# Performance work log

Measured on AMD Instinct MI355X. Metric: run time of the kernel, lower is better.

## Reference

```python
import jax, jax.numpy as jnp
import numpy as np

N_NODES, IN_DIM, HID, LAT, N_EDGES = 50000, 3000, 512, 30, 800000
NEG_SLOPE = 0.2


def setup_inputs() -> dict:
    key = jax.random.key(0)
    ks = jax.random.split(key, 6)
    x = jax.random.normal(ks[0], (N_NODES, IN_DIM), dtype=jnp.float32)
    edge_index = jax.random.randint(ks[1], (2, N_EDGES), 0, N_NODES, dtype=jnp.int64)
    # xavier-normal-ish scales
    W1 = jax.random.normal(ks[2], (IN_DIM, HID), dtype=jnp.float32) * 0.02
    W2 = jax.random.normal(ks[3], (HID, LAT), dtype=jnp.float32) * 0.06
    att_src = jax.random.normal(ks[4], (HID,), dtype=jnp.float32) * 0.1
    att_dst = jax.random.normal(ks[5], (HID,), dtype=jnp.float32) * 0.1
    return {"x": x, "edge_index": edge_index, "W1": W1, "W2": W2,
            "att_src": att_src, "att_dst": att_dst}


def _segment_softmax(e, seg, num_segments):
    # numerically stable softmax over variable-degree dst neighborhoods
    m = jax.ops.segment_max(e, seg, num_segments=num_segments)
    m = jnp.where(jnp.isfinite(m), m, 0.0)  # empty segments -> 0, harmless
    p = jnp.exp(e - m[seg])
    s = jax.ops.segment_sum(p, seg, num_segments=num_segments)
    return p / (s[seg] + 1e-16)


def reference(x, edge_index, W1, W2, att_src, att_dst):
    N = x.shape[0]
    src, dst = edge_index[0], edge_index[1]  # messages flow src(j) -> dst(i)

    # ---- conv1: full GAT layer (heads=1, no self-loops, no bias) ----
    h1 = x @ W1                                   # [N, 512]
    a_src = h1 @ att_src                          # [N]
    a_dst = h1 @ att_dst                          # [N]
    e = jax.nn.leaky_relu(a_src[src] + a_dst[dst], NEG_SLOPE)  # [E]
    alpha = _segment_softmax(e, dst, N)           # [E] (also tied attn for conv3)
    agg1 = jax.ops.segment_sum(h1[src] * alpha[:, None], dst, num_segments=N)
    x1 = jax.nn.elu(agg1)                         # [N, 512]

    # ---- conv2: attention=False -> plain linear projection ----
    x2 = x1 @ W2                                  # [N, 30] (latent embedding)

    # ---- conv3: tied weights (W2^T) + tied attention from conv1 ----
    h3 = x2 @ W2.T                                # [N, 512]
    agg3 = jax.ops.segment_sum(h3[src] * alpha[:, None], dst, num_segments=N)
    x3 = jax.nn.elu(agg3)

    # ---- conv4: attention=False, tied weights (W1^T) ----
    x4 = x3 @ W1.T                                # [N, in_channels]
    return (x2, x4)
```

## Files before the change

### kernel.cpp

```cpp
#include <hip/hip_runtime.h>

#define N_NODES 50000
#define IN_DIM  3000
#define HID     512
#define LAT     30
#define N_EDGES 800000
#define M_PAD   50048
#define K1_PAD  3008
#define N4_PAD  3072

typedef __bf16 bf16;
typedef unsigned int uint;
typedef __attribute__((ext_vector_type(4))) float f32x4;
typedef __attribute__((ext_vector_type(8))) bf16 bf16x8;

__device__ __forceinline__ float bf2f(bf16 b){ return (float)b; }

__device__ __forceinline__ void gl16(const void* g, void* l){
  __builtin_amdgcn_global_load_lds(
      (const __attribute__((address_space(1))) void*)g,
      (__attribute__((address_space(3))) void*)l, 16, 0, 0);
}

__global__ void k_w1t(const float* __restrict__ W1, bf16* __restrict__ W1T){
  int k = blockIdx.x*256 + threadIdx.x;
  int n = blockIdx.y;
  if (k >= K1_PAD) return;
  float v = (k < IN_DIM) ? W1[(long)k*HID + n] : 0.f;
  W1T[(long)n*K1_PAD + k] = (bf16)v;
}
__global__ void k_w1p(const float* __restrict__ W1, bf16* __restrict__ W1P){
  int k = blockIdx.x*256 + threadIdx.x;
  int n = blockIdx.y;
  if (k >= HID) return;
  float v = (n < IN_DIM) ? W1[(long)n*HID + k] : 0.f;
  W1P[(long)n*HID + k] = (bf16)v;
}
__global__ void k_w2t(const float* __restrict__ W2, bf16* __restrict__ W2T){
  int k = blockIdx.x*256 + threadIdx.x;
  int n = blockIdx.y;
  if (k >= HID) return;
  float v = (n < LAT) ? W2[(long)k*LAT + n] : 0.f;
  W2T[(long)n*HID + k] = (bf16)v;
}
__global__ void k_w2p(const float* __restrict__ W2, bf16* __restrict__ W2P){
  int t = blockIdx.x*256 + threadIdx.x;
  if (t >= HID*32) return;
  int n = t >> 5, k = t & 31;
  W2P[t] = (bf16)((k < LAT) ? W2[(long)n*LAT + k] : 0.f);
}

__global__ __launch_bounds__(256) void k_cvt(const float* __restrict__ x, bf16* __restrict__ xb){
  int chunk = blockIdx.x*256 + threadIdx.x;
  int row = blockIdx.y;
  if (chunk >= K1_PAD/8) return;
  int c8 = chunk*8;
  bf16x8 o;
  if (row < N_NODES && c8 + 8 <= IN_DIM){
    float4 v0 = *(const float4*)(x + (long)row*IN_DIM + c8);
    float4 v1 = *(const float4*)(x + (long)row*IN_DIM + c8 + 4);
    o[0]=(bf16)v0.x; o[1]=(bf16)v0.y; o[2]=(bf16)v0.z; o[3]=(bf16)v0.w;
    o[4]=(bf16)v1.x; o[5]=(bf16)v1.y; o[6]=(bf16)v1.z; o[7]=(bf16)v1.w;
  } else {
    #pragma unroll
    for (int j=0;j<8;j++){
      int c = c8 + j;
      float v = (row < N_NODES && c < IN_DIM) ? x[(long)row*IN_DIM + c] : 0.f;
      o[j] = (bf16)v;
    }
  }
  *(bf16x8*)(xb + (long)row*K1_PAD + c8) = o;
}

template<bool C_F32, bool ELU>
__global__ __launch_bounds__(256) void gemm_glds(
    const bf16* __restrict__ A, const bf16* __restrict__ B, void* __restrict__ Cp,
    int lda, int ldb, int Ksteps, int Mvalid, int Nvalid, int ldc)
{
  __shared__ bf16 Alds[128*32];
  __shared__ bf16 Blds[128*32];
  const int tid  = threadIdx.x;
  const int lane = tid & 63;
  const int w    = tid >> 6;
  const int wm   = (w >> 1) * 64, wn = (w & 1) * 64;
  const int col0 = blockIdx.x * 128, row0 = blockIdx.y * 128;

  f32x4 acc[4][4];
  #pragma unroll
  for (int mi=0;mi<4;mi++)
    #pragma unroll
    for (int ni=0;ni<4;ni++)
      acc[mi][ni] = (f32x4){0.f,0.f,0.f,0.f};

  const int sr = tid >> 2;
  const int sc = (tid & 3) * 16;

  const char* ga = (const char*)(A + (long)(row0 + sr) * lda) + sc;
  const char* gb = (const char*)(B + (long)(col0 + sr) * ldb) + sc;
  char* la = (char*)Alds + sr*64 + sc;
  char* lb = (char*)Blds + sr*64 + sc;
  const long astep = (long)64 * lda * 2;
  const long bstep = (long)64 * ldb * 2;

  for (int ks = 0; ks < Ksteps; ks++){
    const long ko = (long)ks * 64;
    gl16(ga + ko,         la);
    gl16(ga + ko + astep, la + 64*64);
    gl16(gb + ko,         lb);
    gl16(gb + ko + bstep, lb + 64*64);
    __syncthreads();

    bf16x8 af[4], bfr[4];
    #pragma unroll
    for (int mi=0;mi<4;mi++)
      af[mi] = *(const bf16x8*)&Alds[(wm + mi*16 + (lane & 15))*32 + (lane>>4)*8];
    #pragma unroll
    for (int ni=0;ni<4;ni++)
      bfr[ni] = *(const bf16x8*)&Blds[(wn + ni*16 + (lane & 15))*32 + (lane>>4)*8];
    #pragma unroll
    for (int mi=0;mi<4;mi++)
      #pragma unroll
      for (int ni=0;ni<4;ni++)
        acc[mi][ni] = __builtin_amdgcn_mfma_f32_16x16x32_bf16(af[mi], bfr[ni], acc[mi][ni], 0, 0, 0);
    __syncthreads();
  }

  const int crb  = (lane >> 4) * 4;
  const int ccol = lane & 15;
  #pragma unroll
  for (int mi=0;mi<4;mi++){
    #pragma unroll
    for (int v=0;v<4;v++){
      int r = row0 + wm + mi*16 + crb + v;
      if (r >= Mvalid) continue;
      #pragma unroll
      for (int ni=0;ni<4;ni++){
        int c = col0 + wn + ni*16 + ccol;
        if (c >= Nvalid) continue;
        float val = acc[mi][ni][v];
        if (ELU) val = (val > 0.f) ? val : expm1f(val);
        if (C_F32) ((float*)Cp)[(long)r*ldc + c] = val;
        else       ((bf16*)Cp)[(long)r*ldc + c] = (bf16)val;
      }
    }
  }
}

__global__ void k_attdots(const bf16* __restrict__ h1, const float* __restrict__ att_s,
                          const float* __restrict__ att_d, float* __restrict__ a_src,
                          float* __restrict__ a_dst){
  int gid = blockIdx.x * blockDim.x + threadIdx.x;
  int row = gid >> 6, lane = gid & 63;
  if (row >= N_NODES) return;
  bf16x8 hv = *(const bf16x8*)(h1 + (long)row*HID + lane*8);
  float s1 = 0.f, s2 = 0.f;
  #pragma unroll
  for (int j=0;j<8;j++){
    float h = bf2f(hv[j]);
    s1 = fmaf(h, att_s[lane*8+j], s1);
    s2 = fmaf(h, att_d[lane*8+j], s2);
  }
  #pragma unroll
  for (int o=32;o>0;o>>=1){ s1 += __shfl_down(s1,o); s2 += __shfl_down(s2,o); }
  if (lane == 0){ a_src[row] = s1; a_dst[row] = s2; }
}

__global__ void k_deg(const int* __restrict__ ei, int* __restrict__ deg){
  int e = blockIdx.x*256 + threadIdx.x;
  if (e >= N_EDGES) return;
  atomicAdd(&deg[ei[N_EDGES + e]], 1);
}

__global__ void k_scan(const int* __restrict__ deg, int* __restrict__ off, int* __restrict__ cur){
  const int n = M_PAD, T = 1024;
  int t = threadIdx.x;
  const int per = (n + T - 1) / T;
  int s0 = t*per, s1 = min(n, s0+per);
  int sum = 0;
  for (int i=s0;i<s1;i++) sum += deg[i];
  __shared__ int sd[1024];
  sd[t] = sum; __syncthreads();
  for (int o=1;o<T;o<<=1){
    int x = (t>=o) ? sd[t-o] : 0;
    __syncthreads();
    sd[t] += x;
    __syncthreads();
  }
  int run = sd[t] - sum;
  for (int i=s0;i<s1;i++){
    off[i] = run; cur[i] = run;
    run += deg[i];
  }
  if (s0 < n && s1 == n) off[n] = run;
}

__global__ void k_fill(const int* __restrict__ ei, int* __restrict__ cur, int* __restrict__ csr_src){
  int e = blockIdx.x*256 + threadIdx.x;
  if (e >= N_EDGES) return;
  int d = ei[N_EDGES + e];
  int pos = atomicAdd(&cur[d], 1);
  csr_src[pos] = ei[e];
}

__global__ __launch_bounds__(512) void k_conv1(
    const int* __restrict__ off, const int* __restrict__ csr_src,
    const float* __restrict__ a_src, const float* __restrict__ a_dst,
    const bf16* __restrict__ h1, bf16* __restrict__ x1,
    float* __restrict__ p_edge, float* __restrict__ s_node)
{
  const int i = blockIdx.x;
  const int t = threadIdx.x;
  const int start = off[i];
  const int deg = off[i+1] - start;
  __shared__ float p_sh[512];
  __shared__ int   s_sh[512];
  __shared__ float red[512];

  const float ad = a_dst[i];
  float mloc = -1e30f;
  for (int base=0; base<deg; base+=512){
    int k = base + t;
    if (k < deg){
      float e = a_src[csr_src[start+k]] + ad;
      e = (e > 0.f) ? e : 0.2f*e;
      mloc = fmaxf(mloc, e);
    }
  }
  red[t] = mloc; __syncthreads();
  for (int o=256;o>0;o>>=1){ if (t<o) red[t] = fmaxf(red[t], red[t+o]); __syncthreads(); }
  const float m = red[0];
  __syncthreads();

  float acc = 0.f, ssum = 0.f;
  for (int base=0; base<deg; base+=512){
    int cnt = min(512, deg-base);
    if (t < cnt){
      int s = csr_src[start+base+t];
      float e = a_src[s] + ad;
      e = (e > 0.f) ? e : 0.2f*e;
      float p = __expf(e - m);
      p_sh[t] = p; s_sh[t] = s;
      p_edge[start+base+t] = p;
    }
    __syncthreads();
    for (int k=0;k<cnt;k++){
      float pk = p_sh[k];
      ssum += pk;
      acc = fmaf(pk, bf2f(h1[(long)s_sh[k]*HID + t]), acc);
    }
    __syncthreads();
  }
  float val = acc / (ssum + 1e-16f);
  val = (val > 0.f) ? val : expm1f(val);
  x1[(long)i*HID + t] = (bf16)val;
  if (t == 0) s_node[i] = ssum;
}

__global__ void k_agg3(const int* __restrict__ off, const int* __restrict__ csr_src,
                       const float* __restrict__ p_edge, const float* __restrict__ s_node,
                       const float* __restrict__ x2, bf16* __restrict__ aggb)
{
  int i = blockIdx.x*8 + (threadIdx.x >> 5);
  int lane = threadIdx.x & 31;
  if (i >= M_PAD) return;
  float acc = 0.f;
  if (i < N_NODES){
    int s0 = off[i], d = off[i+1] - s0;
    for (int k=0;k<d;k++){
      int s = csr_src[s0+k];
      float pk = p_edge[s0+k];
      if (lane < LAT) acc = fmaf(pk, x2[(long)s*LAT + lane], acc);
    }
    acc *= 1.f/(s_node[i] + 1e-16f);
  }
  aggb[(long)i*32 + lane] = (bf16)((lane < LAT) ? acc : 0.f);
}

extern "C" void kernel_launch(void* const* d_in, const int* in_sizes, int n_in,
                              void* d_out, int out_size, void* d_ws, size_t ws_size,
                              hipStream_t stream)
{
  const float* x     = (const float*)d_in[0];
  const int*   ei    = (const int*)d_in[1];
  const float* W1    = (const float*)d_in[2];
  const float* W2    = (const float*)d_in[3];
  const float* att_s = (const float*)d_in[4];
  const float* att_d = (const float*)d_in[5];

  float* out_x2 = (float*)d_out;
  float* out_x4 = (float*)d_out + (long)N_NODES*LAT;

  bf16* xb = (bf16*)out_x4;
  bf16* h1 = xb + (long)M_PAD*K1_PAD;
  bf16* x1 = h1 + (long)M_PAD*HID;

  char* w = (char*)d_ws;
  bf16* W1T = (bf16*)w;  w += (long)HID*K1_PAD*2;
  bf16* W1P = (bf16*)w;  w += (long)N4_PAD*HID*2;
  bf16* W2T = (bf16*)w;  w += (long)128*HID*2;
  bf16* W2P = (bf16*)w;  w += (long)HID*32*2;
  bf16* x3  = (bf16*)w;  w += (long)M_PAD*HID*2;
  bf16* aggb= (bf16*)w;  w += (long)M_PAD*32*2;
  int* deg  = (int*)w;   w += (long)M_PAD*4;
  int* offs = (int*)w;   w += (long)(M_PAD+64)*4;
  int* cur  = (int*)w;   w += (long)M_PAD*4;
  int* csr  = (int*)w;   w += (long)N_EDGES*4;
  float* p_e = (float*)w; w += (long)N_EDGES*4;
  float* s_n = (float*)w; w += (long)M_PAD*4;
  float* a_s = (float*)w; w += (long)M_PAD*4;
  float* a_d = (float*)w; w += (long)M_PAD*4;

  k_w1t<<<dim3((K1_PAD+255)/256, HID), 256, 0, stream>>>(W1, W1T);
  k_w1p<<<dim3((HID+255)/256, N4_PAD), 256, 0, stream>>>(W1, W1P);
  k_w2t<<<dim3(2, 128), 256, 0, stream>>>(W2, W2T);
  k_w2p<<<(HID*32+255)/256, 256, 0, stream>>>(W2, W2P);
  k_cvt<<<dim3((K1_PAD/8+255)/256, M_PAD), 256, 0, stream>>>(x, xb);

  hipMemsetAsync(deg, 0, (size_t)M_PAD*4, stream);
  k_deg<<<(N_EDGES+255)/256, 256, 0, stream>>>(ei, deg);
  k_scan<<<1, 1024, 0, stream>>>(deg, offs, cur);
  k_fill<<<(N_EDGES+255)/256, 256, 0, stream>>>(ei, cur, csr);

  gemm_glds<false,false><<<dim3(HID/128, M_PAD/128), 256, 0, stream>>>(
      xb, W1T, h1, K1_PAD, K1_PAD, K1_PAD/32, M_PAD, HID, HID);

  k_attdots<<<(N_NODES*64)/256, 256, 0, stream>>>(h1, att_s, att_d, a_s, a_d);

  k_conv1<<<M_PAD, 512, 0, stream>>>(offs, csr, a_s, a_d, h1, x1, p_e, s_n);

  gemm_glds<true,false><<<dim3(1, M_PAD/128), 256, 0, stream>>>(
      x1, W2T, out_x2, HID, HID, HID/32, N_NODES, LAT, LAT);

  k_agg3<<<(M_PAD+7)/8, 256, 0, stream>>>(offs, csr, p_e, s_n, out_x2, aggb);
  gemm_glds<false,true><<<dim3(HID/128, M_PAD/128), 256, 0, stream>>>(
      aggb, W2P, x3, 32, 32, 1, M_PAD, HID, HID);

  gemm_glds<true,false><<<dim3(N4_PAD/128, M_PAD/128), 256, 0, stream>>>(
      x3, W1P, out_x4, HID, HID, HID/32, N_NODES, IN_DIM, IN_DIM);
}
```

Baseline: 1.335 ms.

## Fuse fp32-to-bf16 conversion into GEMM1, precompute edge exps, swizzle workgroups across XCDs

```diff
diff --git a/kernel.cpp b/kernel.cpp
--- a/kernel.cpp
+++ b/kernel.cpp
@@ -22,6 +22,12 @@
       (__attribute__((address_space(3))) void*)l, 16, 0, 0);
 }
 
+__device__ __forceinline__ int xcd_swz(int orig, int nwg){
+  int q = nwg >> 3, r = nwg & 7;
+  int xcd = orig & 7, lid = orig >> 3;
+  return (xcd < r ? xcd*(q+1) : r*(q+1) + (xcd-r)*q) + lid;
+}
+
 __global__ void k_w1t(const float* __restrict__ W1, bf16* __restrict__ W1T){
   int k = blockIdx.x*256 + threadIdx.x;
   int n = blockIdx.y;
@@ -50,32 +56,115 @@
   W2P[t] = (bf16)((k < LAT) ? W2[(long)n*LAT + k] : 0.f);
 }
 
-__global__ __launch_bounds__(256) void k_cvt(const float* __restrict__ x, bf16* __restrict__ xb){
-  int chunk = blockIdx.x*256 + threadIdx.x;
-  int row = blockIdx.y;
-  if (chunk >= K1_PAD/8) return;
-  int c8 = chunk*8;
-  bf16x8 o;
-  if (row < N_NODES && c8 + 8 <= IN_DIM){
-    float4 v0 = *(const float4*)(x + (long)row*IN_DIM + c8);
-    float4 v1 = *(const float4*)(x + (long)row*IN_DIM + c8 + 4);
-    o[0]=(bf16)v0.x; o[1]=(bf16)v0.y; o[2]=(bf16)v0.z; o[3]=(bf16)v0.w;
-    o[4]=(bf16)v1.x; o[5]=(bf16)v1.y; o[6]=(bf16)v1.z; o[7]=(bf16)v1.w;
-  } else {
-    #pragma unroll
-    for (int j=0;j<8;j++){
-      int c = c8 + j;
-      float v = (row < N_NODES && c < IN_DIM) ? x[(long)row*IN_DIM + c] : 0.f;
-      o[j] = (bf16)v;
-    }
-  }
-  *(bf16x8*)(xb + (long)row*K1_PAD + c8) = o;
+__global__ __launch_bounds__(256) void gemm_a32(
+    const float* __restrict__ X, const bf16* __restrict__ Bw, bf16* __restrict__ C)
+{
+  __shared__ bf16 Alds[2][128*32];
+  __shared__ bf16 Blds[2][128*32];
+  const int NBX = HID/128;
+  const int tid  = threadIdx.x;
+  const int lane = tid & 63;
+  const int w    = tid >> 6;
+  const int wm   = (w >> 1) * 64, wn = (w & 1) * 64;
+  const int wgid = xcd_swz(blockIdx.x, gridDim.x);
+  const int col0 = (wgid % NBX) * 128, row0 = (wgid / NBX) * 128;
+  const int Ksteps = K1_PAD/32;
+
+  f32x4 acc[4][4];
+  #pragma unroll
+  for (int mi=0;mi<4;mi++)
+    #pragma unroll
+    for (int ni=0;ni<4;ni++)
+      acc[mi][ni] = (f32x4){0.f,0.f,0.f,0.f};
+
+  const int arow = tid >> 1;
+  const int cg   = (tid & 1) * 16;
+  const float* pA = X + (long)min(row0 + arow, N_NODES-1) * IN_DIM;
+
+  const int sr = tid >> 2;
+  const int sc = (tid & 3) * 16;
+  const char* gB = (const char*)(Bw + (long)(col0 + sr) * K1_PAD) + sc;
+  const long bstep = (long)64 * K1_PAD * 2;
+  char* lB0 = (char*)&Blds[0][0] + sr*64 + sc;
+  char* lB1 = (char*)&Blds[1][0] + sr*64 + sc;
+
+  {
+    int kb = cg;
+    float4 q0 = *(const float4*)(pA + kb);
+    float4 q1 = *(const float4*)(pA + kb + 4);
+    float4 q2 = *(const float4*)(pA + kb + 8);
+    float4 q3 = *(const float4*)(pA + kb + 12);
+    gl16(gB, lB0);
+    gl16(gB + bstep, lB0 + 64*64);
+    bf16x8 v0, v1;
+    v0[0]=(bf16)q0.x; v0[1]=(bf16)q0.y; v0[2]=(bf16)q0.z; v0[3]=(bf16)q0.w;
+    v0[4]=(bf16)q1.x; v0[5]=(bf16)q1.y; v0[6]=(bf16)q1.z; v0[7]=(bf16)q1.w;
+    v1[0]=(bf16)q2.x; v1[1]=(bf16)q2.y; v1[2]=(bf16)q2.z; v1[3]=(bf16)q2.w;
+    v1[4]=(bf16)q3.x; v1[5]=(bf16)q3.y; v1[6]=(bf16)q3.z; v1[7]=(bf16)q3.w;
+    *(bf16x8*)&Alds[0][arow*32 + cg]     = v0;
+    *(bf16x8*)&Alds[0][arow*32 + cg + 8] = v1;
+  }
+
+  for (int ks = 0; ks < Ksteps; ks++){
+    const int c = ks & 1;
+    __syncthreads();
+    const bool pf = (ks+1 < Ksteps);
+    float4 q0,q1,q2,q3;
+    if (pf){
+      int kb = (ks+1)*32 + cg;
+      q0 = *(const float4*)(pA + min(kb,      IN_DIM-4));
+      q1 = *(const float4*)(pA + min(kb + 4,  IN_DIM-4));
+      q2 = *(const float4*)(pA + min(kb + 8,  IN_DIM-4));
+      q3 = *(const float4*)(pA + min(kb + 12, IN_DIM-4));
+      const char* g = gB + (long)(ks+1)*64;
+      char* l = c ? lB0 : lB1;
+      gl16(g, l);
+      gl16(g + bstep, l + 64*64);
+    }
+    bf16x8 af[4], bfr[4];
+    #pragma unroll
+    for (int mi=0;mi<4;mi++)
+      af[mi] = *(const bf16x8*)&Alds[c][(wm + mi*16 + (lane & 15))*32 + (lane>>4)*8];
+    #pragma unroll
+    for (int ni=0;ni<4;ni++)
+      bfr[ni] = *(const bf16x8*)&Blds[c][(wn + ni*16 + (lane & 15))*32 + (lane>>4)*8];
+    #pragma unroll
+    for (int mi=0;mi<4;mi++)
+      #pragma unroll
+      for (int ni=0;ni<4;ni++)
+        acc[mi][ni] = __builtin_amdgcn_mfma_f32_16x16x32_bf16(af[mi], bfr[ni], acc[mi][ni], 0, 0, 0);
+    if (pf){
+      bf16x8 v0, v1;
+      v0[0]=(bf16)q0.x; v0[1]=(bf16)q0.y; v0[2]=(bf16)q0.z; v0[3]=(bf16)q0.w;
+      v0[4]=(bf16)q1.x; v0[5]=(bf16)q1.y; v0[6]=(bf16)q1.z; v0[7]=(bf16)q1.w;
+      v1[0]=(bf16)q2.x; v1[1]=(bf16)q2.y; v1[2]=(bf16)q2.z; v1[3]=(bf16)q2.w;
+      v1[4]=(bf16)q3.x; v1[5]=(bf16)q3.y; v1[6]=(bf16)q3.z; v1[7]=(bf16)q3.w;
+      *(bf16x8*)&Alds[c^1][arow*32 + cg]     = v0;
+      *(bf16x8*)&Alds[c^1][arow*32 + cg + 8] = v1;
+    }
+  }
+
+  const int crb  = (lane >> 4) * 4;
+  const int ccol = lane & 15;
+  #pragma unroll
+  for (int mi=0;mi<4;mi++){
+    #pragma unroll
+    for (int v=0;v<4;v++){
+      int r = row0 + wm + mi*16 + crb + v;
+      if (r >= N_NODES) continue;
+      #pragma unroll
+      for (int ni=0;ni<4;ni++){
+        int cc = col0 + wn + ni*16 + ccol;
+        C[(long)r*HID + cc] = (bf16)acc[mi][ni][v];
+      }
+    }
+  }
 }
 
 template<bool C_F32, bool ELU>
 __global__ __launch_bounds__(256) void gemm_glds(
     const bf16* __restrict__ A, const bf16* __restrict__ B, void* __restrict__ Cp,
-    int lda, int ldb, int Ksteps, int Mvalid, int Nvalid, int ldc)
+    int lda, int ldb, int Ksteps, int Mvalid, int Nvalid, int ldc, int NBX)
 {
   __shared__ bf16 Alds[128*32];
   __shared__ bf16 Blds[128*32];
@@ -83,7 +172,8 @@
   const int lane = tid & 63;
   const int w    = tid >> 6;
   const int wm   = (w >> 1) * 64, wn = (w & 1) * 64;
-  const int col0 = blockIdx.x * 128, row0 = blockIdx.y * 128;
+  const int wgid = xcd_swz(blockIdx.x, gridDim.x);
+  const int col0 = (wgid % NBX) * 128, row0 = (wgid / NBX) * 128;
 
   f32x4 acc[4][4];
   #pragma unroll
@@ -194,19 +284,25 @@
   if (s0 < n && s1 == n) off[n] = run;
 }
 
-__global__ void k_fill(const int* __restrict__ ei, int* __restrict__ cur, int* __restrict__ csr_src){
+__global__ void k_fill(const int* __restrict__ ei, int* __restrict__ cur,
+                       int* __restrict__ csr_src, const float* __restrict__ a_s,
+                       const float* __restrict__ a_d, float* __restrict__ p_e){
   int e = blockIdx.x*256 + threadIdx.x;
   if (e >= N_EDGES) return;
+  int s = ei[e];
   int d = ei[N_EDGES + e];
   int pos = atomicAdd(&cur[d], 1);
-  csr_src[pos] = ei[e];
-}
-
-__global__ __launch_bounds__(512) void k_conv1(
+  csr_src[pos] = s;
+  float v = a_s[s] + a_d[d];
+  v = (v > 0.f) ? v : 0.2f*v;
+  p_e[pos] = __expf(v);
+}
+
+__global__ __launch_bounds__(512) void k_agg1(
     const int* __restrict__ off, const int* __restrict__ csr_src,
-    const float* __restrict__ a_src, const float* __restrict__ a_dst,
+    const float* __restrict__ p_edge,
     const bf16* __restrict__ h1, bf16* __restrict__ x1,
-    float* __restrict__ p_edge, float* __restrict__ s_node)
+    float* __restrict__ s_node)
 {
   const int i = blockIdx.x;
   const int t = threadIdx.x;
@@ -214,33 +310,13 @@
   const int deg = off[i+1] - start;
   __shared__ float p_sh[512];
   __shared__ int   s_sh[512];
-  __shared__ float red[512];
-
-  const float ad = a_dst[i];
-  float mloc = -1e30f;
-  for (int base=0; base<deg; base+=512){
-    int k = base + t;
-    if (k < deg){
-      float e = a_src[csr_src[start+k]] + ad;
-      e = (e > 0.f) ? e : 0.2f*e;
-      mloc = fmaxf(mloc, e);
-    }
-  }
-  red[t] = mloc; __syncthreads();
-  for (int o=256;o>0;o>>=1){ if (t<o) red[t] = fmaxf(red[t], red[t+o]); __syncthreads(); }
-  const float m = red[0];
-  __syncthreads();
 
   float acc = 0.f, ssum = 0.f;
   for (int base=0; base<deg; base+=512){
     int cnt = min(512, deg-base);
     if (t < cnt){
-      int s = csr_src[start+base+t];
-      float e = a_src[s] + ad;
-      e = (e > 0.f) ? e : 0.2f*e;
-      float p = __expf(e - m);
-      p_sh[t] = p; s_sh[t] = s;
-      p_edge[start+base+t] = p;
+      p_sh[t] = p_edge[start+base+t];
+      s_sh[t] = csr_src[start+base+t];
     }
     __syncthreads();
     for (int k=0;k<cnt;k++){
@@ -290,8 +366,7 @@
   float* out_x2 = (float*)d_out;
   float* out_x4 = (float*)d_out + (long)N_NODES*LAT;
 
-  bf16* xb = (bf16*)out_x4;
-  bf16* h1 = xb + (long)M_PAD*K1_PAD;
+  bf16* h1 = (bf16*)out_x4;
   bf16* x1 = h1 + (long)M_PAD*HID;
 
   char* w = (char*)d_ws;
@@ -314,27 +389,26 @@
   k_w1p<<<dim3((HID+255)/256, N4_PAD), 256, 0, stream>>>(W1, W1P);
   k_w2t<<<dim3(2, 128), 256, 0, stream>>>(W2, W2T);
   k_w2p<<<(HID*32+255)/256, 256, 0, stream>>>(W2, W2P);
-  k_cvt<<<dim3((K1_PAD/8+255)/256, M_PAD), 256, 0, stream>>>(x, xb);
 
   hipMemsetAsync(deg, 0, (size_t)M_PAD*4, stream);
   k_deg<<<(N_EDGES+255)/256, 256, 0, stream>>>(ei, deg);
   k_scan<<<1, 1024, 0, stream>>>(deg, offs, cur);
-  k_fill<<<(N_EDGES+255)/256, 256, 0, stream>>>(ei, cur, csr);
-
-  gemm_glds<false,false><<<dim3(HID/128, M_PAD/128), 256, 0, stream>>>(
-      xb, W1T, h1, K1_PAD, K1_PAD, K1_PAD/32, M_PAD, HID, HID);
+
+  gemm_a32<<<(M_PAD/128)*(HID/128), 256, 0, stream>>>(x, W1T, h1);
 
   k_attdots<<<(N_NODES*64)/256, 256, 0, stream>>>(h1, att_s, att_d, a_s, a_d);
 
-  k_conv1<<<M_PAD, 512, 0, stream>>>(offs, csr, a_s, a_d, h1, x1, p_e, s_n);
-
-  gemm_glds<true,false><<<dim3(1, M_PAD/128), 256, 0, stream>>>(
-      x1, W2T, out_x2, HID, HID, HID/32, N_NODES, LAT, LAT);
+  k_fill<<<(N_EDGES+255)/256, 256, 0, stream>>>(ei, cur, csr, a_s, a_d, p_e);
+
+  k_agg1<<<N_NODES, 512, 0, stream>>>(offs, csr, p_e, h1, x1, s_n);
+
+  gemm_glds<true,false><<<1*(M_PAD/128), 256, 0, stream>>>(
+      x1, W2T, out_x2, HID, HID, HID/32, N_NODES, LAT, LAT, 1);
 
   k_agg3<<<(M_PAD+7)/8, 256, 0, stream>>>(offs, csr, p_e, s_n, out_x2, aggb);
-  gemm_glds<false,true><<<dim3(HID/128, M_PAD/128), 256, 0, stream>>>(
-      aggb, W2P, x3, 32, 32, 1, M_PAD, HID, HID);
-
-  gemm_glds<true,false><<<dim3(N4_PAD/128, M_PAD/128), 256, 0, stream>>>(
-      x3, W1P, out_x4, HID, HID, HID/32, N_NODES, IN_DIM, IN_DIM);
-}
+  gemm_glds<false,true><<<(HID/128)*(M_PAD/128), 256, 0, stream>>>(
+      aggb, W2P, x3, 32, 32, 1, M_PAD, HID, HID, HID/128);
+
+  gemm_glds<true,false><<<(N4_PAD/128)*(M_PAD/128), 256, 0, stream>>>(
+      x3, W1P, out_x4, HID, HID, HID/32, N_NODES, IN_DIM, IN_DIM, N4_PAD/128);
+}
```

New measurement: 1.362 ms. 2.1% more time.

## Double-buffer GEMM LDS loads, swizzle XCD tiles, precompute edge exps in fill

Applied to the files above, without the earlier changes.

```diff
diff --git a/kernel.cpp b/kernel.cpp
--- a/kernel.cpp
+++ b/kernel.cpp
@@ -20,6 +20,12 @@
   __builtin_amdgcn_global_load_lds(
       (const __attribute__((address_space(1))) void*)g,
       (__attribute__((address_space(3))) void*)l, 16, 0, 0);
+}
+
+__device__ __forceinline__ int xcd_swz(int orig, int nwg){
+  int q = nwg >> 3, r = nwg & 7;
+  int xcd = orig & 7, lid = orig >> 3;
+  return (xcd < r ? xcd*(q+1) : r*(q+1) + (xcd-r)*q) + lid;
 }
 
 __global__ void k_w1t(const float* __restrict__ W1, bf16* __restrict__ W1T){
@@ -75,15 +81,16 @@
 template<bool C_F32, bool ELU>
 __global__ __launch_bounds__(256) void gemm_glds(
     const bf16* __restrict__ A, const bf16* __restrict__ B, void* __restrict__ Cp,
-    int lda, int ldb, int Ksteps, int Mvalid, int Nvalid, int ldc)
+    int lda, int ldb, int Ksteps, int Mvalid, int Nvalid, int ldc, int NBX)
 {
-  __shared__ bf16 Alds[128*32];
-  __shared__ bf16 Blds[128*32];
+  __shared__ bf16 Alds[2][128*32];
+  __shared__ bf16 Blds[2][128*32];
   const int tid  = threadIdx.x;
   const int lane = tid & 63;
   const int w    = tid >> 6;
   const int wm   = (w >> 1) * 64, wn = (w & 1) * 64;
-  const int col0 = blockIdx.x * 128, row0 = blockIdx.y * 128;
+  const int wgid = xcd_swz(blockIdx.x, gridDim.x);
+  const int col0 = (wgid % NBX) * 128, row0 = (wgid / NBX) * 128;
 
   f32x4 acc[4][4];
   #pragma unroll
@@ -94,36 +101,51 @@
 
   const int sr = tid >> 2;
   const int sc = (tid & 3) * 16;
-
   const char* ga = (const char*)(A + (long)(row0 + sr) * lda) + sc;
   const char* gb = (const char*)(B + (long)(col0 + sr) * ldb) + sc;
-  char* la = (char*)Alds + sr*64 + sc;
-  char* lb = (char*)Blds + sr*64 + sc;
   const long astep = (long)64 * lda * 2;
   const long bstep = (long)64 * ldb * 2;
 
+#define STAGE_G(buf, ks) do{                                            \
+    const long ko_ = (long)(ks) * 64;                                   \
+    char* la_ = (char*)&Alds[buf][0] + sr*64 + sc;                      \
+    char* lb_ = (char*)&Blds[buf][0] + sr*64 + sc;                      \
+    gl16(ga + ko_,         la_);                                        \
+    gl16(ga + ko_ + astep, la_ + 64*64);                                \
+    gl16(gb + ko_,         lb_);                                        \
+    gl16(gb + ko_ + bstep, lb_ + 64*64);                                \
+  }while(0)
+
+  STAGE_G(0, 0);
+
   for (int ks = 0; ks < Ksteps; ks++){
-    const long ko = (long)ks * 64;
-    gl16(ga + ko,         la);
-    gl16(ga + ko + astep, la + 64*64);
-    gl16(gb + ko,         lb);
-    gl16(gb + ko + bstep, lb + 64*64);
-    __syncthreads();
-
+    const int cur = ks & 1;
+    if (ks + 1 < Ksteps){
+      STAGE_G(cur^1, ks+1);
+      asm volatile("s_waitcnt vmcnt(4)" ::: "memory");
+    } else {
+      asm volatile("s_waitcnt vmcnt(0)" ::: "memory");
+    }
+    __builtin_amdgcn_s_barrier();
+
+    const bf16* Ac = &Alds[cur][0];
+    const bf16* Bc = &Blds[cur][0];
     bf16x8 af[4], bfr[4];
     #pragma unroll
     for (int mi=0;mi<4;mi++)
-      af[mi] = *(const bf16x8*)&Alds[(wm + mi*16 + (lane & 15))*32 + (lane>>4)*8];
+      af[mi] = *(const bf16x8*)&Ac[(wm + mi*16 + (lane & 15))*32 + (lane>>4)*8];
     #pragma unroll
     for (int ni=0;ni<4;ni++)
-      bfr[ni] = *(const bf16x8*)&Blds[(wn + ni*16 + (lane & 15))*32 + (lane>>4)*8];
+      bfr[ni] = *(const bf16x8*)&Bc[(wn + ni*16 + (lane & 15))*32 + (lane>>4)*8];
     #pragma unroll
     for (int mi=0;mi<4;mi++)
       #pragma unroll
       for (int ni=0;ni<4;ni++)
         acc[mi][ni] = __builtin_amdgcn_mfma_f32_16x16x32_bf16(af[mi], bfr[ni], acc[mi][ni], 0, 0, 0);
-    __syncthreads();
-  }
+
+    __builtin_amdgcn_s_barrier();
+  }
+#undef STAGE_G
 
   const int crb  = (lane >> 4) * 4;
   const int ccol = lane & 15;
@@ -194,19 +216,25 @@
   if (s0 < n && s1 == n) off[n] = run;
 }
 
-__global__ void k_fill(const int* __restrict__ ei, int* __restrict__ cur, int* __restrict__ csr_src){
+__global__ void k_fill(const int* __restrict__ ei, int* __restrict__ cur,
+                       int* __restrict__ csr_src, const float* __restrict__ a_s,
+                       const float* __restrict__ a_d, float* __restrict__ p_e){
   int e = blockIdx.x*256 + threadIdx.x;
   if (e >= N_EDGES) return;
+  int s = ei[e];
   int d = ei[N_EDGES + e];
   int pos = atomicAdd(&cur[d], 1);
-  csr_src[pos] = ei[e];
-}
-
-__global__ __launch_bounds__(512) void k_conv1(
+  csr_src[pos] = s;
+  float v = a_s[s] + a_d[d];
+  v = (v > 0.f) ? v : 0.2f*v;
+  p_e[pos] = __expf(v);
+}
+
+__global__ __launch_bounds__(512) void k_agg1(
     const int* __restrict__ off, const int* __restrict__ csr_src,
-    const float* __restrict__ a_src, const float* __restrict__ a_dst,
+    const float* __restrict__ p_edge,
     const bf16* __restrict__ h1, bf16* __restrict__ x1,
-    float* __restrict__ p_edge, float* __restrict__ s_node)
+    float* __restrict__ s_node)
 {
   const int i = blockIdx.x;
   const int t = threadIdx.x;
@@ -214,33 +242,13 @@
   const int deg = off[i+1] - start;
   __shared__ float p_sh[512];
   __shared__ int   s_sh[512];
-  __shared__ float red[512];
-
-  const float ad = a_dst[i];
-  float mloc = -1e30f;
-  for (int base=0; base<deg; base+=512){
-    int k = base + t;
-    if (k < deg){
-      float e = a_src[csr_src[start+k]] + ad;
-      e = (e > 0.f) ? e : 0.2f*e;
-      mloc = fmaxf(mloc, e);
-    }
-  }
-  red[t] = mloc; __syncthreads();
-  for (int o=256;o>0;o>>=1){ if (t<o) red[t] = fmaxf(red[t], red[t+o]); __syncthreads(); }
-  const float m = red[0];
-  __syncthreads();
 
   float acc = 0.f, ssum = 0.f;
   for (int base=0; base<deg; base+=512){
     int cnt = min(512, deg-base);
     if (t < cnt){
-      int s = csr_src[start+base+t];
-      float e = a_src[s] + ad;
-      e = (e > 0.f) ? e : 0.2f*e;
-      float p = __expf(e - m);
-      p_sh[t] = p; s_sh[t] = s;
-      p_edge[start+base+t] = p;
+      p_sh[t] = p_edge[start+base+t];
+      s_sh[t] = csr_src[start+base+t];
     }
     __syncthreads();
     for (int k=0;k<cnt;k++){
@@ -319,22 +327,23 @@
   hipMemsetAsync(deg, 0, (size_t)M_PAD*4, stream);
   k_deg<<<(N_EDGES+255)/256, 256, 0, stream>>>(ei, deg);
   k_scan<<<1, 1024, 0, stream>>>(deg, offs, cur);
-  k_fill<<<(N_EDGES+255)/256, 256, 0, stream>>>(ei, cur, csr);
-
-  gemm_glds<false,false><<<dim3(HID/128, M_PAD/128), 256, 0, stream>>>(
-      xb, W1T, h1, K1_PAD, K1_PAD, K1_PAD/32, M_PAD, HID, HID);
+
+  gemm_glds<false,false><<<(HID/128)*(M_PAD/128), 256, 0, stream>>>(
+      xb, W1T, h1, K1_PAD, K1_PAD, K1_PAD/32, N_NODES, HID, HID, HID/128);
 
   k_attdots<<<(N_NODES*64)/256, 256, 0, stream>>>(h1, att_s, att_d, a_s, a_d);
 
-  k_conv1<<<M_PAD, 512, 0, stream>>>(offs, csr, a_s, a_d, h1, x1, p_e, s_n);
-
-  gemm_glds<true,false><<<dim3(1, M_PAD/128), 256, 0, stream>>>(
-      x1, W2T, out_x2, HID, HID, HID/32, N_NODES, LAT, LAT);
+  k_fill<<<(N_EDGES+255)/256, 256, 0, stream>>>(ei, cur, csr, a_s, a_d, p_e);
+
+  k_agg1<<<N_NODES, 512, 0, stream>>>(offs, csr, p_e, h1, x1, s_n);
+
+  gemm_glds<true,false><<<1*(M_PAD/128), 256, 0, stream>>>(
+      x1, W2T, out_x2, HID, HID, HID/32, N_NODES, LAT, LAT, 1);
 
   k_agg3<<<(M_PAD+7)/8, 256, 0, stream>>>(offs, csr, p_e, s_n, out_x2, aggb);
-  gemm_glds<false,true><<<dim3(HID/128, M_PAD/128), 256, 0, stream>>>(
-      aggb, W2P, x3, 32, 32, 1, M_PAD, HID, HID);
-
-  gemm_glds<true,false><<<dim3(N4_PAD/128, M_PAD/128), 256, 0, stream>>>(
-      x3, W1P, out_x4, HID, HID, HID/32, N_NODES, IN_DIM, IN_DIM);
-}
+  gemm_glds<false,true><<<(HID/128)*(M_PAD/128), 256, 0, stream>>>(
+      aggb, W2P, x3, 32, 32, 1, M_PAD, HID, HID, HID/128);
+
+  gemm_glds<true,false><<<(N4_PAD/128)*(M_PAD/128), 256, 0, stream>>>(
+      x3, W1P, out_x4, HID, HID, HID/32, N_NODES, IN_DIM, IN_DIM, N4_PAD/128);
+}
```

Measured after the change: 1.211 ms. -9.3%, faster.
